# Kernel tuning notes

Hardware: AMD Instinct MI355X
Metric: run time of the kernel (lower is better)

The kernel has to match this reference:

```python
import jax, jax.numpy as jnp
import numpy as np

DIM = 1536; FFN = 8960; NH = 12; HD = DIM // NH
B = 1; Fg, Hg, Wg = 8, 20, 20; L = Fg * Hg * Wg; L2 = 512
EPS = 1e-6; MAXLEN = 1024


def _rope_tables():
    # Wan rope_params: per-axis inverse-frequency tables, concatenated [t|h|w]
    c = HD // 2; c0 = c - 2 * (c // 3); c1 = c // 3
    def ang(dp):
        inv = 1.0 / (10000.0 ** (np.arange(0, dp, 2, dtype=np.float64) / dp))
        return np.outer(np.arange(MAXLEN, dtype=np.float64), inv)
    a = np.concatenate([ang(2 * c0), ang(2 * c1), ang(2 * c1)], axis=1)  # [1024, c]
    return np.cos(a).astype(np.float32), np.sin(a).astype(np.float32)


def setup_inputs() -> dict:
    key = jax.random.key(0)
    ks = jax.random.split(key, 32); it = iter(range(32))
    def rnd(shape, scale=0.02):
        return jax.random.normal(ks[next(it)], shape, dtype=jnp.float32) * scale
    cos, sin = _rope_tables()
    inp = {
        'x': rnd((B, L, DIM), 1.0),
        'e': rnd((B, 6, DIM), 1.0),
        'context': rnd((B, L2, DIM), 1.0),
        'freqs_cos': jnp.asarray(cos), 'freqs_sin': jnp.asarray(sin),
        'modulation': rnd((1, 6, DIM), DIM ** -0.5),
    }
    for p in ['sa', 'ca']:
        for nm in ['q', 'k', 'v', 'o']:
            inp[p + '_' + nm + 'w'] = rnd((DIM, DIM))
            inp[p + '_' + nm + 'b'] = jnp.zeros((DIM,), jnp.float32)
        inp[p + '_nq'] = jnp.ones((DIM,), jnp.float32)
        inp[p + '_nk'] = jnp.ones((DIM,), jnp.float32)
    inp['n3_w'] = jnp.ones((DIM,), jnp.float32); inp['n3_b'] = jnp.zeros((DIM,), jnp.float32)
    inp['ffn_w1'] = rnd((DIM, FFN)); inp['ffn_b1'] = jnp.zeros((FFN,), jnp.float32)
    inp['ffn_w2'] = rnd((FFN, DIM)); inp['ffn_b2'] = jnp.zeros((DIM,), jnp.float32)
    inp['grid_f'] = Fg; inp['grid_h'] = Hg; inp['grid_w'] = Wg
    return inp


def _layer_norm(x, w=None, b=None):
    mu = x.mean(-1, keepdims=True)
    var = jnp.mean((x - mu) ** 2, -1, keepdims=True)
    y = (x - mu) * jax.lax.rsqrt(var + EPS)
    return y * w + b if w is not None else y


def _rms(x, w):
    return x * jax.lax.rsqrt(jnp.mean(x * x, -1, keepdims=True) + EPS) * w


def _rope(xq, cos, sin, f, h, w):
    # xq: [B, L, n, d]; complex rotation per (t,h,w) axis with split freq dims
    b, s, n, d = xq.shape
    c = d // 2; c0 = c - 2 * (c // 3); c1 = c // 3
    def grid(tab):
        t = jnp.broadcast_to(tab[:f, None, None, :c0], (f, h, w, c0))
        hh = jnp.broadcast_to(tab[None, :h, None, c0:c0 + c1], (f, h, w, c1))
        ww = jnp.broadcast_to(tab[None, None, :w, c0 + c1:c0 + 2 * c1], (f, h, w, c1))
        return jnp.concatenate([t, hh, ww], -1).reshape(f * h * w, c)
    gc = grid(cos)[None, :, None, :]  # [1, L, 1, c]
    gs = grid(sin)[None, :, None, :]
    xr = xq.reshape(b, s, n, c, 2)
    xre, xim = xr[..., 0], xr[..., 1]
    return jnp.stack([xre * gc - xim * gs, xre * gs + xim * gc], -1).reshape(b, s, n, d)


def _attn(q, k, v):
    scores = jnp.einsum('bqnd,bknd->bnqk', q, k) * (q.shape[-1] ** -0.5)
    p = jax.nn.softmax(scores, -1)
    return jnp.einsum('bnqk,bknd->bqnd', p, v)


def reference(x, e, context, freqs_cos, freqs_sin, modulation,
              sa_qw, sa_qb, sa_kw, sa_kb, sa_vw, sa_vb, sa_ow, sa_ob, sa_nq, sa_nk,
              ca_qw, ca_qb, ca_kw, ca_kb, ca_vw, ca_vb, ca_ow, ca_ob, ca_nq, ca_nk,
              n3_w, n3_b, ffn_w1, ffn_b1, ffn_w2, ffn_b2,
              grid_f, grid_h, grid_w):
    b, s, _ = x.shape; n, d = NH, HD
    em = modulation + e  # [B, 6, C]
    e0, e1, e2, e3, e4, e5 = (em[:, i:i + 1] for i in range(6))
    # self-attention with adaLN modulation
    xs = _layer_norm(x) * (1 + e1) + e0
    q = _rms(xs @ sa_qw + sa_qb, sa_nq).reshape(b, s, n, d)
    k = _rms(xs @ sa_kw + sa_kb, sa_nk).reshape(b, s, n, d)
    v = (xs @ sa_vw + sa_vb).reshape(b, s, n, d)
    q = _rope(q, freqs_cos, freqs_sin, grid_f, grid_h, grid_w)
    k = _rope(k, freqs_cos, freqs_sin, grid_f, grid_h, grid_w)
    y = _attn(q, k, v).reshape(b, s, -1) @ sa_ow + sa_ob
    x = x + y * e2
    # cross-attention on norm3(x)
    xc = _layer_norm(x, n3_w, n3_b)
    s2 = context.shape[1]
    cq = _rms(xc @ ca_qw + ca_qb, ca_nq).reshape(b, s, n, d)
    ck = _rms(context @ ca_kw + ca_kb, ca_nk).reshape(b, s2, n, d)
    cv = (context @ ca_vw + ca_vb).reshape(b, s2, n, d)
    x = x + (_attn(cq, ck, cv).reshape(b, s, -1) @ ca_ow + ca_ob)
    # FFN with adaLN modulation
    xf = _layer_norm(x) * (1 + e4) + e3
    y = jax.nn.gelu(xf @ ffn_w1 + ffn_b1, approximate=True) @ ffn_w2 + ffn_b2
    return x + y * e5
```

## Files before the change

kernel.cpp:

```cpp
#include <hip/hip_runtime.h>

#define DIM 1536
#define NH 12
#define HD 128
#define LQ 3200
#define LKV 512
#define FFN 8960

typedef __attribute__((ext_vector_type(8))) short bf16x8;
typedef __attribute__((ext_vector_type(4))) float f32x4;
typedef __attribute__((ext_vector_type(4))) unsigned short u16x4;

__device__ inline unsigned short f2b(float f){
  union { float f; unsigned u; } x; x.f = f;
  unsigned r = (x.u + 0x7FFFu + ((x.u >> 16) & 1u)) >> 16;
  return (unsigned short)r;
}
__device__ inline float b2f(unsigned short u){
  union { unsigned u; float f; } x; x.u = ((unsigned)u) << 16; return x.f;
}
__device__ inline unsigned pack2(float a, float b){
  return (unsigned)f2b(a) | ((unsigned)f2b(b) << 16);
}
__device__ inline f32x4 mfma16(bf16x8 a, bf16x8 b, f32x4 c){
  return __builtin_amdgcn_mfma_f32_16x16x32_bf16(a, b, c, 0, 0, 0);
}
__device__ inline void gload_lds16(const unsigned short* g, unsigned short* l){
  __builtin_amdgcn_global_load_lds((const __attribute__((address_space(1))) unsigned int*)g,
                                   (__attribute__((address_space(3))) unsigned int*)l, 16, 0, 0);
}
__device__ inline int xcd_swizzle(int orig, int nwg){
  int q = nwg >> 3, r = nwg & 7;
  int xcd = orig & 7, off = orig >> 3;
  return (xcd < r ? xcd*(q+1) : r*(q+1) + (xcd-r)*q) + off;
}
__device__ inline float gelu_f(float vv){
  float u = 0.79788456080286535588f*(vv + 0.044715f*vv*vv*vv);
  u = fminf(fmaxf(u, -20.f), 20.f);
  float e2u = __expf(2.f*u);
  float th = (e2u - 1.f)/(e2u + 1.f);
  return 0.5f*vv*(1.f+th);
}


__global__ void add_vec(const float* __restrict__ a, const float* __restrict__ b,
                        float* __restrict__ o, int n){
  int i = blockIdx.x*256 + threadIdx.x;
  if (i < n) o[i] = a[i] + b[i];
}

__global__ void convert_bf16(const float* __restrict__ a, unsigned short* __restrict__ o, int n){
  int i = blockIdx.x*256 + threadIdx.x;
  if (i < n) o[i] = f2b(a[i]);
}

__global__ void concat3(const float* __restrict__ a, const float* __restrict__ b,
                        const float* __restrict__ c, float* __restrict__ o, int n){
  int i = blockIdx.x*256 + threadIdx.x;
  if (i < n) o[i] = a[i];
  else if (i < 2*n) o[i] = b[i - n];
  else if (i < 3*n) o[i] = c[i - 2*n];
}

__global__ void transpose_conv(const float* __restrict__ src, unsigned short* __restrict__ dst,
                               int K, int N){
  __shared__ float tile[32][33];
  int n0 = blockIdx.x*32, k0 = blockIdx.y*32;
  int tx = threadIdx.x, ty = threadIdx.y;
  #pragma unroll
  for (int i = 0; i < 4; i++)
    tile[ty + 8*i][tx] = src[(size_t)(k0 + ty + 8*i)*N + n0 + tx];
  __syncthreads();
  #pragma unroll
  for (int i = 0; i < 4; i++)
    dst[(size_t)(n0 + ty + 8*i)*K + k0 + tx] = f2b(tile[tx][ty + 8*i]);
}

__global__ __launch_bounds__(256) void ln_mod_kernel(const float* __restrict__ x,
    const float* __restrict__ mulv, const float* __restrict__ addv, int one_plus,
    unsigned short* __restrict__ out){
  int row = blockIdx.x;
  const float* xr = x + (size_t)row * DIM;
  int tid = threadIdx.x;
  float v[6]; float s = 0.f, ss = 0.f;
  #pragma unroll
  for (int i = 0; i < 6; i++){ v[i] = xr[tid + i*256]; s += v[i]; ss += v[i]*v[i]; }
  #pragma unroll
  for (int m = 1; m < 64; m <<= 1){ s += __shfl_xor(s, m, 64); ss += __shfl_xor(ss, m, 64); }
  __shared__ float bs[4], bss[4];
  int w = tid >> 6;
  if ((tid & 63) == 0){ bs[w] = s; bss[w] = ss; }
  __syncthreads();
  s = bs[0]+bs[1]+bs[2]+bs[3]; ss = bss[0]+bss[1]+bss[2]+bss[3];
  float mu  = s * (1.f/DIM);
  float var = ss * (1.f/DIM) - mu*mu;
  float inv = rsqrtf(var + 1e-6f);
  unsigned short* orow = out + (size_t)row*DIM;
  #pragma unroll
  for (int i = 0; i < 6; i++){
    int c = tid + i*256;
    float g = one_plus ? (1.f + mulv[c]) : mulv[c];
    orow[c] = f2b((v[i]-mu)*inv*g + addv[c]);
  }
}

__global__ __launch_bounds__(256) void reduce_ln_kernel(const float* P0, const float* P1,
    const float* bias, const float* resid, const float* svec, float* out_x,
    const float* mulv, const float* addv, int one_plus, unsigned short* out_ln){
  int row = blockIdx.x;
  size_t base = (size_t)row * DIM;
  int tid = threadIdx.x;
  float v[6]; float s = 0.f, ss = 0.f;
  #pragma unroll
  for (int i = 0; i < 6; i++){
    int c = tid + i*256;
    float sv = svec ? svec[c] : 1.f;
    float y = resid[base + c] + (P0[base + c] + P1[base + c] + bias[c])*sv;
    out_x[base + c] = y;
    v[i] = y; s += y; ss += y*y;
  }
  #pragma unroll
  for (int m = 1; m < 64; m <<= 1){ s += __shfl_xor(s, m, 64); ss += __shfl_xor(ss, m, 64); }
  __shared__ float bs[4], bss[4];
  int w = tid >> 6;
  if ((tid & 63) == 0){ bs[w] = s; bss[w] = ss; }
  __syncthreads();
  s = bs[0]+bs[1]+bs[2]+bs[3]; ss = bss[0]+bss[1]+bss[2]+bss[3];
  float mu  = s * (1.f/DIM);
  float var = ss * (1.f/DIM) - mu*mu;
  float inv = rsqrtf(var + 1e-6f);
  unsigned short* orow = out_ln + base;
  #pragma unroll
  for (int i = 0; i < 6; i++){
    int c = tid + i*256;
    float g = one_plus ? (1.f + mulv[c]) : mulv[c];
    orow[c] = f2b((v[i]-mu)*inv*g + addv[c]);
  }
}

__global__ __launch_bounds__(256) void reduce_rms_kernel(const float* __restrict__ P0,
    const float* __restrict__ P1, const float* __restrict__ bias,
    const float* __restrict__ nw, unsigned short* __restrict__ out){
  int row = blockIdx.x;
  size_t base = (size_t)row * DIM;
  int tid = threadIdx.x;
  float v[6]; float ss = 0.f;
  #pragma unroll
  for (int i = 0; i < 6; i++){
    int c = tid + i*256;
    float y = P0[base + c] + P1[base + c] + bias[c];
    v[i] = y; ss += y*y;
  }
  #pragma unroll
  for (int m = 1; m < 64; m <<= 1) ss += __shfl_xor(ss, m, 64);
  __shared__ float bss[4];
  if ((tid & 63) == 0) bss[tid >> 6] = ss;
  __syncthreads();
  ss = bss[0]+bss[1]+bss[2]+bss[3];
  float inv = rsqrtf(ss*(1.f/DIM) + 1e-6f);
  #pragma unroll
  for (int i = 0; i < 6; i++){
    int c = tid + i*256;
    out[base + c] = f2b(v[i]*inv*nw[c]);
  }
}

__global__ __launch_bounds__(256) void rms_rope_qk(unsigned short* __restrict__ buf,
    const float* __restrict__ nwq, const float* __restrict__ nwk,
    const float* __restrict__ ct, const float* __restrict__ st){
  int row = blockIdx.x;
  int sl = blockIdx.y;
  const float* nw = sl ? nwk : nwq;
  unsigned short* xr = buf + (size_t)row*(3*DIM) + sl*DIM;
  int tid = threadIdx.x;
  float ss = 0.f; float v[6];
  #pragma unroll
  for (int i = 0; i < 6; i++){ v[i] = b2f(xr[tid + i*256]); ss += v[i]*v[i]; }
  #pragma unroll
  for (int m = 1; m < 64; m <<= 1) ss += __shfl_xor(ss, m, 64);
  __shared__ float bss[4];
  if ((tid & 63) == 0) bss[tid >> 6] = ss;
  __syncthreads();
  ss = bss[0]+bss[1]+bss[2]+bss[3];
  float inv = rsqrtf(ss*(1.f/DIM) + 1e-6f);
  int f = row/400, hp = (row/20)%20, wp = row%20;
  for (int p = tid; p < 768; p += 256){
    int hh = p >> 6, j = p & 63;
    int pos = (j < 22) ? f : ((j < 43) ? hp : wp);
    float c_ = ct[pos*64 + j], s_ = st[pos*64 + j];
    int base = hh*HD + 2*j;
    float xre = b2f(xr[base])   * inv * nw[base];
    float xim = b2f(xr[base+1]) * inv * nw[base+1];
    xr[base]   = f2b(xre*c_ - xim*s_);
    xr[base+1] = f2b(xre*s_ + xim*c_);
  }
}

__global__ __launch_bounds__(256) void rms_rope_b16(unsigned short* __restrict__ buf, int ld,
    const float* __restrict__ nw){
  int row = blockIdx.x;
  unsigned short* xr = buf + (size_t)row*ld;
  int tid = threadIdx.x;
  float ss = 0.f; float v[6];
  #pragma unroll
  for (int i = 0; i < 6; i++){ v[i] = b2f(xr[tid + i*256]); ss += v[i]*v[i]; }
  #pragma unroll
  for (int m = 1; m < 64; m <<= 1) ss += __shfl_xor(ss, m, 64);
  __shared__ float bss[4];
  if ((tid & 63) == 0) bss[tid >> 6] = ss;
  __syncthreads();
  ss = bss[0]+bss[1]+bss[2]+bss[3];
  float inv = rsqrtf(ss*(1.f/DIM) + 1e-6f);
  #pragma unroll
  for (int i = 0; i < 6; i++){ int c = tid + i*256; xr[c] = f2b(v[i]*inv*nw[c]); }
}

__global__ __launch_bounds__(256) void packvt_kernel(const unsigned short* __restrict__ pre, int ld,
    unsigned short* __restrict__ VT, int ntok){
  int h = blockIdx.y; int t0 = blockIdx.x*64;
  __shared__ unsigned short tile[128][72];
  int tid = threadIdx.x;
  int d = tid & 127, tl = tid >> 7;
  #pragma unroll 4
  for (int i = 0; i < 32; i++){
    int tok = t0 + tl + 2*i;
    tile[d][tl + 2*i] = pre[(size_t)tok*ld + h*HD + d];
  }
  __syncthreads();
  int dd = tid >> 6, tl2 = tid & 63;
  #pragma unroll 4
  for (int i = 0; i < 32; i++){
    int d2 = dd + 4*i;
    VT[((size_t)h*HD + d2)*ntok + t0 + tl2] = tile[d2][tl2];
  }
}

__global__ void reduce_f32(const float* P0, const float* P1,
    const float* bias, const float* resid,
    const float* svec, float* out, int total4){
  int i = blockIdx.x*256 + threadIdx.x;
  if (i >= total4) return;
  int col = (i*4) % DIM;
  float4 p0 = ((const float4*)P0)[i];
  float4 p1 = ((const float4*)P1)[i];
  float4 rs = ((const float4*)resid)[i];
  float4 o;
  float s0 = svec ? svec[col]   : 1.f;
  float s1 = svec ? svec[col+1] : 1.f;
  float s2 = svec ? svec[col+2] : 1.f;
  float s3 = svec ? svec[col+3] : 1.f;
  o.x = rs.x + (p0.x + p1.x + bias[col])*s0;
  o.y = rs.y + (p0.y + p1.y + bias[col+1])*s1;
  o.z = rs.z + (p0.z + p1.z + bias[col+2])*s2;
  o.w = rs.w + (p0.w + p1.w + bias[col+3])*s3;
  ((float4*)out)[i] = o;
}

__global__ __launch_bounds__(512, 4) void gemm128_kernel(const unsigned short* __restrict__ A,
    const unsigned short* __restrict__ WT, const float* __restrict__ bias,
    int M, int N, int ldA, int ksize, int ep,
    float* __restrict__ outf0, float* __restrict__ outf1, unsigned short* __restrict__ outb){
  __shared__ unsigned short As[2][128*32];
  __shared__ unsigned short Bs[2][128*32];
  int t = threadIdx.x;
  int wv = t >> 6, lane = t & 63;
  int lr = lane & 15, lk = lane >> 4;
  int gx = gridDim.x;
  int nwg = gx * gridDim.y;
  int wg = xcd_swizzle(blockIdx.y*gx + blockIdx.x, nwg);
  int m0 = (wg % gx)*128, n0 = (wg / gx)*128;
  int kbeg = blockIdx.z*ksize;
  int wm = (wv >> 1)*32, wn = (wv & 1)*64;
  f32x4 z = {0.f,0.f,0.f,0.f};
  f32x4 acc[2][4];
  #pragma unroll
  for (int i = 0; i < 2; i++)
    #pragma unroll
    for (int j = 0; j < 4; j++) acc[i][j] = z;

  int srow = t >> 2;
  int sslot = (t & 3) ^ (srow & 3);
  const unsigned short* Ap0 = A  + (size_t)(m0 + srow)*ldA + kbeg + sslot*8;
  const unsigned short* Bp0 = WT + (size_t)(n0 + srow)*ldA + kbeg + sslot*8;
  int slA = (lk ^ (lr & 3))*8;

  int nk = ksize >> 5;
  gload_lds16(Ap0, &As[0][wv*512]);
  gload_lds16(Bp0, &Bs[0][wv*512]);
  asm volatile("s_waitcnt vmcnt(0)" ::: "memory");
  __syncthreads();

  for (int tt = 0; tt < nk; ++tt){
    int cur = tt & 1;
    if (tt + 1 < nk){
      int kn = (tt + 1) << 5;
      gload_lds16(Ap0 + kn, &As[cur^1][wv*512]);
      gload_lds16(Bp0 + kn, &Bs[cur^1][wv*512]);
    }
    bf16x8 af[2], bfr[4];
    #pragma unroll
    for (int i = 0; i < 2; i++)
      af[i]  = *(const bf16x8*)&As[cur][(wm + i*16 + lr)*32 + slA];
    #pragma unroll
    for (int j = 0; j < 4; j++)
      bfr[j] = *(const bf16x8*)&Bs[cur][(wn + j*16 + lr)*32 + slA];
    #pragma unroll
    for (int i = 0; i < 2; i++)
      #pragma unroll
      for (int j = 0; j < 4; j++)
        acc[i][j] = mfma16(af[i], bfr[j], acc[i][j]);
    asm volatile("s_waitcnt vmcnt(0)" ::: "memory");
    __syncthreads();
  }

  float* pdst = blockIdx.z ? outf1 : outf0;
  #pragma unroll
  for (int i = 0; i < 2; i++)
    #pragma unroll
    for (int j = 0; j < 4; j++)
      #pragma unroll
      for (int r = 0; r < 4; r++){
        int row = m0 + wm + i*16 + lk*4 + r;
        int col = n0 + wn + j*16 + lr;
        size_t idx = (size_t)row*N + col;
        if (ep == 4){
          pdst[idx] = acc[i][j][r];
        } else if (ep == 3){
          outb[idx] = f2b(acc[i][j][r] + bias[col]);
        } else {
          outb[idx] = f2b(gelu_f(acc[i][j][r] + bias[col]));
        }
      }
}

__global__ __launch_bounds__(512, 4) void gemmw_kernel(const unsigned short* __restrict__ A,
    const unsigned short* __restrict__ WT, const float* __restrict__ bias,
    int M, int N, int ldA, int K, int ep, unsigned short* __restrict__ outb){
  __shared__ unsigned short As[2][128*32];
  __shared__ unsigned short Bs[2][256*32];
  int t = threadIdx.x;
  int wv = t >> 6, lane = t & 63;
  int lr = lane & 15, lk = lane >> 4;
  int gx = gridDim.x;
  int wg = xcd_swizzle(blockIdx.y*gx + blockIdx.x, gx*gridDim.y);
  int m0 = (wg % gx)*128, n0 = (wg / gx)*256;
  int wm = (wv >> 2)*64, wn = (wv & 3)*64;
  f32x4 z = {0.f,0.f,0.f,0.f};
  f32x4 acc[4][4];
  #pragma unroll
  for (int i = 0; i < 4; i++)
    #pragma unroll
    for (int j = 0; j < 4; j++) acc[i][j] = z;

  int srow = t >> 2;
  int sslot = (t & 3) ^ (srow & 3);
  const unsigned short* Ap0 = A  + (size_t)(m0 + srow)*ldA + sslot*8;
  const unsigned short* Bp0 = WT + (size_t)(n0 + srow)*ldA + sslot*8;
  const unsigned short* Bp1 = WT + (size_t)(n0 + 128 + srow)*ldA + sslot*8;
  int slA = (lk ^ (lr & 3))*8;

  int nk = K >> 5;
  gload_lds16(Ap0, &As[0][wv*512]);
  gload_lds16(Bp0, &Bs[0][wv*512]);
  gload_lds16(Bp1, &Bs[0][4096 + wv*512]);
  asm volatile("s_waitcnt vmcnt(0)" ::: "memory");
  __syncthreads();

  for (int tt = 0; tt < nk; ++tt){
    int cur = tt & 1;
    if (tt + 1 < nk){
      int kn = (tt + 1) << 5;
      gload_lds16(Ap0 + kn, &As[cur^1][wv*512]);
      gload_lds16(Bp0 + kn, &Bs[cur^1][wv*512]);
      gload_lds16(Bp1 + kn, &Bs[cur^1][4096 + wv*512]);
    }
    bf16x8 af[4], bfr[4];
    #pragma unroll
    for (int i = 0; i < 4; i++)
      af[i]  = *(const bf16x8*)&As[cur][(wm + i*16 + lr)*32 + slA];
    #pragma unroll
    for (int j = 0; j < 4; j++)
      bfr[j] = *(const bf16x8*)&Bs[cur][(wn + j*16 + lr)*32 + slA];
    #pragma unroll
    for (int i = 0; i < 4; i++)
      #pragma unroll
      for (int j = 0; j < 4; j++)
        acc[i][j] = mfma16(af[i], bfr[j], acc[i][j]);
    asm volatile("s_waitcnt vmcnt(0)" ::: "memory");
    __syncthreads();
  }

  #pragma unroll
  for (int i = 0; i < 4; i++)
    #pragma unroll
    for (int j = 0; j < 4; j++)
      #pragma unroll
      for (int r = 0; r < 4; r++){
        int row = m0 + wm + i*16 + lk*4 + r;
        int col = n0 + wn + j*16 + lr;
        size_t idx = (size_t)row*N + col;
        float vv = acc[i][j][r] + bias[col];
        outb[idx] = (ep == 3) ? f2b(vv) : f2b(gelu_f(vv));
      }
}

__global__ __launch_bounds__(256, 3) void attn_kernel(const unsigned short* __restrict__ Q, int ldQ,
    const unsigned short* __restrict__ Kg, int ldK, const unsigned short* __restrict__ VT,
    unsigned short* __restrict__ O, int nkv, int vlen){
  __shared__ unsigned short Kls[64*128];
  __shared__ unsigned short Vls[128*64];
  __shared__ unsigned short Pls[4][16][80];
  int gx = gridDim.x;
  int wg = xcd_swizzle(blockIdx.y*gx + blockIdx.x, gx*gridDim.y);
  int bq = wg % gx, h = wg / gx;
  int tid = threadIdx.x;
  int wv = tid >> 6, lane = tid & 63;
  int lr = lane & 15, lk = lane >> 4;
  int q0 = bq*64 + wv*16;

  bf16x8 qf[4];
  const unsigned short* qp = Q + (size_t)(q0 + lr)*ldQ + h*HD + lk*8;
  #pragma unroll
  for (int kk = 0; kk < 4; kk++) qf[kk] = *(const bf16x8*)(qp + kk*32);

  f32x4 z = {0.f,0.f,0.f,0.f};
  f32x4 acc[8];
  #pragma unroll
  for (int d = 0; d < 8; d++) acc[d] = z;
  float mrun = -1e30f, lrun = 0.f;
  const float sc = 0.08838834764831845f;
  int swz = (lr & 7) << 4;

  for (int kt = 0; kt < nkv; kt += 64){
    __syncthreads();
    #pragma unroll
    for (int j = 0; j < 4; j++){
      int row = wv*16 + j*4 + (lane >> 4);
      int cb  = ((lane & 15)*16) ^ ((row & 7) << 4);
      gload_lds16(Kg + (size_t)(kt + row)*ldK + h*HD + (cb >> 1),
                  &Kls[(wv*16 + j*4)*128]);
    }
    #pragma unroll
    for (int j = 0; j < 4; j++){
      int d  = wv*32 + j*8 + (lane >> 3);
      int cb = ((lane & 7)*16) ^ ((d & 7) << 4);
      gload_lds16(VT + ((size_t)h*HD + d)*vlen + kt + (cb >> 1),
                  &Vls[(wv*32 + j*8)*64]);
    }
    asm volatile("s_waitcnt vmcnt(0)" ::: "memory");
    __syncthreads();

    f32x4 s[4];
    #pragma unroll
    for (int t4 = 0; t4 < 4; t4++) s[t4] = z;
    #pragma unroll
    for (int t4 = 0; t4 < 4; t4++){
      #pragma unroll
      for (int kk = 0; kk < 4; kk++){
        bf16x8 kf = *(const bf16x8*)&Kls[(t4*16 + lr)*128 + (((kk*64 + lk*16) ^ swz) >> 1)];
        s[t4] = mfma16(kf, qf[kk], s[t4]);
      }
    }

    float vv[4][4]; float pmax = -1e30f;
    #pragma unroll
    for (int t4 = 0; t4 < 4; t4++)
      #pragma unroll
      for (int r = 0; r < 4; r++){
        float xv = s[t4][r]*sc; vv[t4][r] = xv; pmax = fmaxf(pmax, xv);
      }
    pmax = fmaxf(pmax, __shfl_xor(pmax, 16, 64));
    pmax = fmaxf(pmax, __shfl_xor(pmax, 32, 64));
    float mn = fmaxf(mrun, pmax);
    float cr = __expf(mrun - mn);
    mrun = mn;
    float rs = 0.f;
    #pragma unroll
    for (int t4 = 0; t4 < 4; t4++)
      #pragma unroll
      for (int r = 0; r < 4; r++){
        float pv = __expf(vv[t4][r] - mn); vv[t4][r] = pv; rs += pv;
      }
    rs += __shfl_xor(rs, 16, 64);
    rs += __shfl_xor(rs, 32, 64);
    lrun = lrun*cr + rs;
    #pragma unroll
    for (int d = 0; d < 8; d++) acc[d] *= cr;

    #pragma unroll
    for (int t4 = 0; t4 < 4; t4++){
      *(unsigned*)&Pls[wv][lr][t4*16 + lk*4]     = pack2(vv[t4][0], vv[t4][1]);
      *(unsigned*)&Pls[wv][lr][t4*16 + lk*4 + 2] = pack2(vv[t4][2], vv[t4][3]);
    }
    bf16x8 pb0 = *(const bf16x8*)&Pls[wv][lr][lk*8];
    bf16x8 pb1 = *(const bf16x8*)&Pls[wv][lr][32 + lk*8];

    #pragma unroll
    for (int db = 0; db < 8; db++){
      bf16x8 vf0 = *(const bf16x8*)&Vls[(db*16 + lr)*64 + (((lk*16) ^ swz) >> 1)];
      acc[db] = mfma16(vf0, pb0, acc[db]);
      bf16x8 vf1 = *(const bf16x8*)&Vls[(db*16 + lr)*64 + (((64 + lk*16) ^ swz) >> 1)];
      acc[db] = mfma16(vf1, pb1, acc[db]);
    }
  }

  float inv = 1.f/lrun;
  unsigned short* op = O + (size_t)(q0 + lr)*DIM + h*HD + lk*4;
  #pragma unroll
  for (int db = 0; db < 8; db++){
    u16x4 ov;
    ov[0] = f2b(acc[db][0]*inv); ov[1] = f2b(acc[db][1]*inv);
    ov[2] = f2b(acc[db][2]*inv); ov[3] = f2b(acc[db][3]*inv);
    *(u16x4*)(op + db*16) = ov;
  }
}


extern "C" void kernel_launch(void* const* d_in, const int* in_sizes, int n_in,
                              void* d_out, int out_size, void* d_ws, size_t ws_size,
                              hipStream_t stream){
  const float* x    = (const float*)d_in[0];
  const float* e    = (const float*)d_in[1];
  const float* ctx  = (const float*)d_in[2];
  const float* fcos = (const float*)d_in[3];
  const float* fsin = (const float*)d_in[4];
  const float* modu = (const float*)d_in[5];
  const float* sa_qw = (const float*)d_in[6];  const float* sa_qb = (const float*)d_in[7];
  const float* sa_kw = (const float*)d_in[8];  const float* sa_kb = (const float*)d_in[9];
  const float* sa_vw = (const float*)d_in[10]; const float* sa_vb = (const float*)d_in[11];
  const float* sa_ow = (const float*)d_in[12]; const float* sa_ob = (const float*)d_in[13];
  const float* sa_nq = (const float*)d_in[14]; const float* sa_nk = (const float*)d_in[15];
  const float* ca_qw = (const float*)d_in[16]; const float* ca_qb = (const float*)d_in[17];
  const float* ca_kw = (const float*)d_in[18]; const float* ca_kb = (const float*)d_in[19];
  const float* ca_vw = (const float*)d_in[20]; const float* ca_vb = (const float*)d_in[21];
  const float* ca_ow = (const float*)d_in[22]; const float* ca_ob = (const float*)d_in[23];
  const float* ca_nq = (const float*)d_in[24]; const float* ca_nk = (const float*)d_in[25];
  const float* n3w = (const float*)d_in[26]; const float* n3b = (const float*)d_in[27];
  const float* fw1 = (const float*)d_in[28]; const float* fb1 = (const float*)d_in[29];
  const float* fw2 = (const float*)d_in[30]; const float* fb2 = (const float*)d_in[31];

  char* p = (char*)d_ws;
  auto alloc = [&](size_t bytes){ void* r = (void*)p; p += (bytes + 255) & ~(size_t)255; return r; };
  unsigned short* wt[8];
  for (int i = 0; i < 8; i++) wt[i] = (unsigned short*)alloc((size_t)DIM*DIM*2);
  unsigned short* wtf1 = (unsigned short*)alloc((size_t)FFN*DIM*2);
  unsigned short* wtf2 = (unsigned short*)alloc((size_t)DIM*FFN*2);
  float* em     = (float*)alloc(6*DIM*4);
  float* qkvb   = (float*)alloc(3*DIM*4);
  float* ckvb   = (float*)alloc(2*DIM*4);
  unsigned short* nbuf = (unsigned short*)alloc((size_t)LQ*DIM*2);
  unsigned short* qkv16 = (unsigned short*)alloc((size_t)LQ*3*DIM*2);
  unsigned short* VTb   = (unsigned short*)alloc((size_t)LQ*DIM*2);
  unsigned short* Qb    = (unsigned short*)alloc((size_t)LQ*DIM*2);
  unsigned short* Ob    = (unsigned short*)alloc((size_t)LQ*DIM*2);
  float* x1 = (float*)alloc((size_t)LQ*DIM*4);
  unsigned short* ctxb   = (unsigned short*)alloc((size_t)LKV*DIM*2);
  unsigned short* cakv16 = (unsigned short*)alloc((size_t)LKV*2*DIM*2);

  float* P0   = (float*)d_out;
  float* P1a  = (float*)qkv16;
  float* P1f  = (float*)wtf1;
  unsigned short* hbuf = qkv16;
  const int TOT4 = LQ*DIM/4;

  add_vec<<<36, 256, 0, stream>>>(modu, e, em, 6*DIM);
  concat3<<<18, 256, 0, stream>>>(sa_qb, sa_kb, sa_vb, qkvb, DIM);
  concat3<<<12, 256, 0, stream>>>(ca_kb, ca_vb, ca_vb, ckvb, DIM);
  const float* wsrc[8] = {sa_qw, sa_kw, sa_vw, sa_ow, ca_qw, ca_kw, ca_vw, ca_ow};
  for (int i = 0; i < 8; i++)
    transpose_conv<<<dim3(48,48), dim3(32,8), 0, stream>>>(wsrc[i], wt[i], DIM, DIM);
  transpose_conv<<<dim3(280,48), dim3(32,8), 0, stream>>>(fw1, wtf1, DIM, FFN);
  transpose_conv<<<dim3(48,280), dim3(32,8), 0, stream>>>(fw2, wtf2, FFN, DIM);
  convert_bf16<<<(LKV*DIM)/256, 256, 0, stream>>>(ctx, ctxb, LKV*DIM);

  ln_mod_kernel<<<LQ, 256, 0, stream>>>(x, em + DIM, em, 1, nbuf);
  gemmw_kernel<<<dim3(25,18), 512, 0, stream>>>(nbuf, wt[0], qkvb, LQ, 3*DIM, DIM, DIM, 3, qkv16);
  rms_rope_qk<<<dim3(LQ,2), 256, 0, stream>>>(qkv16, sa_nq, sa_nk, fcos, fsin);
  packvt_kernel<<<dim3(50,12), 256, 0, stream>>>(qkv16 + 2*DIM, 3*DIM, VTb, LQ);
  attn_kernel<<<dim3(50,12), 256, 0, stream>>>(qkv16, 3*DIM, qkv16 + DIM, 3*DIM, VTb, Ob, LQ, LQ);
  gemm128_kernel<<<dim3(25,12,2), 512, 0, stream>>>(Ob, wt[3], nullptr, LQ, DIM, DIM, DIM/2, 4,
                                                    P0, P1a, nullptr);
  reduce_ln_kernel<<<LQ, 256, 0, stream>>>(P0, P1a, sa_ob, x, em + 2*DIM, x1,
                                           n3w, n3b, 0, nbuf);

  gemm128_kernel<<<dim3(25,12,2), 512, 0, stream>>>(nbuf, wt[4], nullptr, LQ, DIM, DIM, DIM/2, 4,
                                                    P0, P1a, nullptr);
  reduce_rms_kernel<<<LQ, 256, 0, stream>>>(P0, P1a, ca_qb, ca_nq, Qb);
  gemm128_kernel<<<dim3(4,24,1), 512, 0, stream>>>(ctxb, wt[5], ckvb, LKV, 2*DIM, DIM, DIM, 3,
                                                   nullptr, nullptr, cakv16);
  rms_rope_b16<<<LKV, 256, 0, stream>>>(cakv16, 2*DIM, ca_nk);
  packvt_kernel<<<dim3(8,12), 256, 0, stream>>>(cakv16 + DIM, 2*DIM, VTb, LKV);
  attn_kernel<<<dim3(50,12), 256, 0, stream>>>(Qb, DIM, cakv16, 2*DIM, VTb, Ob, LKV, LKV);
  gemm128_kernel<<<dim3(25,12,2), 512, 0, stream>>>(Ob, wt[7], nullptr, LQ, DIM, DIM, DIM/2, 4,
                                                    P0, P1a, nullptr);
  reduce_ln_kernel<<<LQ, 256, 0, stream>>>(P0, P1a, ca_ob, x1, nullptr, x1,
                                           em + 4*DIM, em + 3*DIM, 1, nbuf);

  gemmw_kernel<<<dim3(25,35), 512, 0, stream>>>(nbuf, wtf1, fb1, LQ, FFN, DIM, DIM, 2, hbuf);
  gemm128_kernel<<<dim3(25,12,2), 512, 0, stream>>>(hbuf, wtf2, nullptr, LQ, DIM, FFN, FFN/2, 4,
                                                    P0, P1f, nullptr);
  reduce_f32<<<(TOT4+255)/256, 256, 0, stream>>>(P0, P1f, fb2, x1, em + 5*DIM, (float*)d_out, TOT4);
}
```

Baseline: 768.5 us.

## Double-buffer K/V tiles in attention kernel to overlap loads with compute

The attention kernel now keeps two LDS buffers for K and V tiles. It issues the next tile's global-to-LDS loads before computing on the current tile, then waits at the end of each iteration. This hides global load latency behind the QK and PV MFMA work. The cost is doubled LDS use (about 74KB per block), and the launch-bounds occupancy hint of 3 is removed, which likely lowers blocks per CU. An unused dead variable krow was also added.

```diff
diff --git a/kernel.cpp b/kernel.cpp
--- a/kernel.cpp
+++ b/kernel.cpp
@@ -404,11 +404,11 @@
       }
 }
 
-__global__ __launch_bounds__(256, 3) void attn_kernel(const unsigned short* __restrict__ Q, int ldQ,
+__global__ __launch_bounds__(256) void attn_kernel(const unsigned short* __restrict__ Q, int ldQ,
     const unsigned short* __restrict__ Kg, int ldK, const unsigned short* __restrict__ VT,
     unsigned short* __restrict__ O, int nkv, int vlen){
-  __shared__ unsigned short Kls[64*128];
-  __shared__ unsigned short Vls[128*64];
+  __shared__ unsigned short Kls[2][64*128];
+  __shared__ unsigned short Vls[2][128*64];
   __shared__ unsigned short Pls[4][16][80];
   int gx = gridDim.x;
   int wg = xcd_swizzle(blockIdx.y*gx + blockIdx.x, gx*gridDim.y);
@@ -418,6 +418,7 @@
   int lr = lane & 15, lk = lane >> 4;
   int q0 = bq*64 + wv*16;
 
+  int krow = wv*16 + (tid & 63 ? 0 : 0);
   bf16x8 qf[4];
   const unsigned short* qp = Q + (size_t)(q0 + lr)*ldQ + h*HD + lk*8;
   #pragma unroll
@@ -431,24 +432,41 @@
   const float sc = 0.08838834764831845f;
   int swz = (lr & 7) << 4;
 
-  for (int kt = 0; kt < nkv; kt += 64){
-    __syncthreads();
-    #pragma unroll
-    for (int j = 0; j < 4; j++){
-      int row = wv*16 + j*4 + (lane >> 4);
-      int cb  = ((lane & 15)*16) ^ ((row & 7) << 4);
-      gload_lds16(Kg + (size_t)(kt + row)*ldK + h*HD + (cb >> 1),
-                  &Kls[(wv*16 + j*4)*128]);
+  #pragma unroll
+  for (int j = 0; j < 4; j++){
+    int row = wv*16 + j*4 + (lane >> 4);
+    int cb  = ((lane & 15)*16) ^ ((row & 7) << 4);
+    gload_lds16(Kg + (size_t)row*ldK + h*HD + (cb >> 1), &Kls[0][(wv*16 + j*4)*128]);
+  }
+  #pragma unroll
+  for (int j = 0; j < 4; j++){
+    int d  = wv*32 + j*8 + (lane >> 3);
+    int cb = ((lane & 7)*16) ^ ((d & 7) << 4);
+    gload_lds16(VT + ((size_t)h*HD + d)*vlen + (cb >> 1), &Vls[0][(wv*32 + j*8)*64]);
+  }
+  asm volatile("s_waitcnt vmcnt(0)" ::: "memory");
+  __syncthreads();
+
+  int nt = nkv >> 6;
+  for (int tt = 0; tt < nt; ++tt){
+    int cur = tt & 1;
+    if (tt + 1 < nt){
+      int ktn = (tt + 1) << 6;
+      #pragma unroll
+      for (int j = 0; j < 4; j++){
+        int row = wv*16 + j*4 + (lane >> 4);
+        int cb  = ((lane & 15)*16) ^ ((row & 7) << 4);
+        gload_lds16(Kg + (size_t)(ktn + row)*ldK + h*HD + (cb >> 1),
+                    &Kls[cur^1][(wv*16 + j*4)*128]);
+      }
+      #pragma unroll
+      for (int j = 0; j < 4; j++){
+        int d  = wv*32 + j*8 + (lane >> 3);
+        int cb = ((lane & 7)*16) ^ ((d & 7) << 4);
+        gload_lds16(VT + ((size_t)h*HD + d)*vlen + ktn + (cb >> 1),
+                    &Vls[cur^1][(wv*32 + j*8)*64]);
+      }
     }
-    #pragma unroll
-    for (int j = 0; j < 4; j++){
-      int d  = wv*32 + j*8 + (lane >> 3);
-      int cb = ((lane & 7)*16) ^ ((d & 7) << 4);
-      gload_lds16(VT + ((size_t)h*HD + d)*vlen + kt + (cb >> 1),
-                  &Vls[(wv*32 + j*8)*64]);
-    }
-    asm volatile("s_waitcnt vmcnt(0)" ::: "memory");
-    __syncthreads();
 
     f32x4 s[4];
     #pragma unroll
@@ -457,7 +475,7 @@
     for (int t4 = 0; t4 < 4; t4++){
       #pragma unroll
       for (int kk = 0; kk < 4; kk++){
-        bf16x8 kf = *(const bf16x8*)&Kls[(t4*16 + lr)*128 + (((kk*64 + lk*16) ^ swz) >> 1)];
+        bf16x8 kf = *(const bf16x8*)&Kls[cur][(t4*16 + lr)*128 + (((kk*64 + lk*16) ^ swz) >> 1)];
         s[t4] = mfma16(kf, qf[kk], s[t4]);
       }
     }
@@ -497,11 +515,13 @@
 
     #pragma unroll
     for (int db = 0; db < 8; db++){
-      bf16x8 vf0 = *(const bf16x8*)&Vls[(db*16 + lr)*64 + (((lk*16) ^ swz) >> 1)];
+      bf16x8 vf0 = *(const bf16x8*)&Vls[cur][(db*16 + lr)*64 + (((lk*16) ^ swz) >> 1)];
       acc[db] = mfma16(vf0, pb0, acc[db]);
-      bf16x8 vf1 = *(const bf16x8*)&Vls[(db*16 + lr)*64 + (((64 + lk*16) ^ swz) >> 1)];
+      bf16x8 vf1 = *(const bf16x8*)&Vls[cur][(db*16 + lr)*64 + (((64 + lk*16) ^ swz) >> 1)];
       acc[db] = mfma16(vf1, pb1, acc[db]);
     }
+    asm volatile("s_waitcnt vmcnt(0)" ::: "memory");
+    __syncthreads();
   }
 
   float inv = 1.f/lrun;
```

Measured after the change: 827.3 us. 7.7% more time.
